# Kernel optimization log

Hardware: AMD Instinct MI355X
Metric: run time of the kernel (lower is better)

The kernel has to match this reference:

```python
import jax, jax.numpy as jnp
import numpy as np

N_NODES = 10000
DEG = 32          # random neighbors per node; +1 self loop (A + I in original)
BATCH = 2
F_IN = 128
D_EMB = 128


def _make_edges():
    # np.where on a dense (A+I) matrix yields edges sorted by source row;
    # we build the same sorted-by-src edge list directly.
    rng = np.random.default_rng(0)
    src = np.repeat(np.arange(N_NODES), DEG + 1)
    dst = rng.integers(0, N_NODES, size=N_NODES * (DEG + 1))
    dst[DEG::DEG + 1] = np.arange(N_NODES)  # guarantee self loops
    return np.stack([src, dst], axis=1).astype(np.int32)  # [E, 2]


def setup_inputs() -> dict:
    key = jax.random.key(0)
    k1, k2, k3 = jax.random.split(key, 3)
    inputs = jax.random.normal(k1, (BATCH, N_NODES, F_IN), jnp.float32)
    W = jax.random.normal(k2, (F_IN, D_EMB), jnp.float32) * 0.1
    W_attn = jax.random.normal(k3, (2 * D_EMB, 1), jnp.float32) * 0.1
    edges = jnp.asarray(_make_edges())
    return {"inputs": inputs, "W": W, "W_attn": W_attn, "edges": edges}


def reference(inputs, W, W_attn, edges):
    # inputs: [B, N, F]; W: [F, D]; W_attn: [2D, 1]; edges: [E, 2] (sorted by src)
    B, N, _ = inputs.shape
    D = W.shape[1]
    src, dst = edges[:, 0], edges[:, 1]

    h = inputs @ W  # [B, N, D] node_states_transformed

    # Original: gather [src,dst] feats, reshape to [B,E,2D], matmul W_attn.
    # Equivalent efficient form: split W_attn and project per node first.
    a_src, a_dst = W_attn[:D, 0], W_attn[D:, 0]
    s = h @ a_src  # [B, N]
    d = h @ a_dst  # [B, N]
    scores = jax.nn.leaky_relu(s[:, src] + d[:, dst], negative_slope=0.2)  # [B, E]
    scores = jnp.exp(jnp.clip(scores, -2.0, 2.0))

    # Faithful to original bug: denominator uses batch 0 only, shared across batch.
    denom = jax.ops.segment_sum(scores[0], src, num_segments=N)  # [N]
    # edges sorted by src => tf.repeat(denom, bincount(src)) == denom[src]
    attn = scores / denom[src][None, :]  # [B, E]

    msgs = h[:, dst] * attn[:, :, None]  # [B, E, D]
    # tf.unsorted_segment_sum with rank-2 segment_ids sums over batch AND edges.
    out = jax.ops.segment_sum(msgs.sum(axis=0), src, num_segments=N)  # [N, D]
    return jnp.broadcast_to(out[None], (B, N, D))
```

## Files before the change

kernel.cpp:

```cpp
#include <hip/hip_runtime.h>
#include <math.h>

#define N_NODES 10000
#define DEG1 33
#define D_EMB 128
#define F_IN 128
#define BATCH 2

typedef short s8v  __attribute__((ext_vector_type(8)));
typedef float f4v  __attribute__((ext_vector_type(4)));

static __device__ __forceinline__ unsigned short f2bf(float f) {
    unsigned int x = __float_as_uint(f);
    unsigned int r = (x + 0x7fffu + ((x >> 16) & 1u)) >> 16;
    return (unsigned short)r;
}
static __device__ __forceinline__ float rdlane_f(float v, int l) {
    return __uint_as_float((unsigned int)__builtin_amdgcn_readlane((int)__float_as_uint(v), l));
}

__global__ __launch_bounds__(256) void gat_prep_kernel(
    const float* __restrict__ W, unsigned short* __restrict__ wtf)
{
    const int c = blockIdx.x;
    const int t = threadIdx.x;
    __shared__ float xs[128 * 16];
    #pragma unroll
    for (int r = 0; r < 8; ++r) {
        const int k = r * 16 + (t >> 4);
        const int n = t & 15;
        xs[k * 16 + n] = W[k * 128 + c * 16 + n];
    }
    __syncthreads();
    const int s = t >> 6;
    const int l = t & 63;
    s8v frag;
    #pragma unroll
    for (int j = 0; j < 8; ++j) {
        const int k = s * 32 + (l >> 4) * 8 + j;
        frag[j] = (short)f2bf(xs[k * 16 + (l & 15)]);
    }
    *(s8v*)&wtf[(((size_t)c * 4 + s) * 64 + l) * 8] = frag;
}

__global__ __launch_bounds__(256) void gat_h_kernel(
    const float* __restrict__ X, const unsigned short* __restrict__ wtf,
    const float* __restrict__ Wattn,
    unsigned char* __restrict__ hb8, float* __restrict__ pk4, float* __restrict__ s2)
{
    __shared__ float lds_sd[2][2][2][16];
    __shared__ float lds_mx[2][2][16];
    const int wave = threadIdx.x >> 6;
    const int lane = threadIdx.x & 63;
    const int quad = lane >> 4;
    const int mrow = lane & 15;
    const int rg   = wave >> 1;
    const int half = wave & 1;
    const int row0 = (blockIdx.x * 2 + rg) * 16;

    f4v acc[4];
    #pragma unroll
    for (int cc = 0; cc < 4; ++cc) acc[cc] = (f4v){0.f, 0.f, 0.f, 0.f};

    const float* xrow = X + (size_t)(row0 + mrow) * F_IN;
    #pragma unroll
    for (int s = 0; s < 4; ++s) {
        const int k0 = s * 32 + quad * 8;
        const float4 xa = *(const float4*)&xrow[k0];
        const float4 xbv = *(const float4*)&xrow[k0 + 4];
        s8v a;
        a[0] = (short)f2bf(xa.x);  a[1] = (short)f2bf(xa.y);
        a[2] = (short)f2bf(xa.z);  a[3] = (short)f2bf(xa.w);
        a[4] = (short)f2bf(xbv.x); a[5] = (short)f2bf(xbv.y);
        a[6] = (short)f2bf(xbv.z); a[7] = (short)f2bf(xbv.w);
        #pragma unroll
        for (int cc = 0; cc < 4; ++cc) {
            const int c = half * 4 + cc;
            const s8v b = *(const s8v*)&wtf[(((size_t)c * 4 + s) * 64 + lane) * 8];
            acc[cc] = __builtin_amdgcn_mfma_f32_16x16x32_bf16(a, b, acc[cc], 0, 0, 0);
        }
    }

    float as[4], ad[4];
    #pragma unroll
    for (int cc = 0; cc < 4; ++cc) {
        as[cc] = Wattn[(half * 4 + cc) * 16 + mrow];
        ad[cc] = Wattn[D_EMB + (half * 4 + cc) * 16 + mrow];
    }
    #pragma unroll
    for (int r = 0; r < 4; ++r) {
        float sv = 0.f, dv = 0.f, mx = 0.f;
        #pragma unroll
        for (int cc = 0; cc < 4; ++cc) {
            sv = fmaf(acc[cc][r], as[cc], sv);
            dv = fmaf(acc[cc][r], ad[cc], dv);
            mx = fmaxf(mx, fabsf(acc[cc][r]));
        }
        #pragma unroll
        for (int off = 1; off < 16; off <<= 1) {
            sv += __shfl_xor(sv, off, 16);
            dv += __shfl_xor(dv, off, 16);
            mx = fmaxf(mx, __shfl_xor(mx, off, 16));
        }
        if (mrow == 0) {
            lds_sd[rg][half][0][quad * 4 + r] = sv;
            lds_sd[rg][half][1][quad * 4 + r] = dv;
            lds_mx[rg][half][quad * 4 + r] = mx;
        }
    }
    __syncthreads();

    const int b = (row0 >= N_NODES) ? 1 : 0;
    #pragma unroll
    for (int r = 0; r < 4; ++r) {
        const int qr = quad * 4 + r;
        const float mx = fmaxf(fmaxf(lds_mx[rg][0][qr], lds_mx[rg][1][qr]), 1e-20f);
        const float inv_s = 127.f / mx;
        const int n = (row0 + qr) - b * N_NODES;
        unsigned char* dst = &hb8[((size_t)n * 2 + b) * D_EMB + half * 64 + mrow];
        #pragma unroll
        for (int cc = 0; cc < 4; ++cc) {
            const float tq = fminf(fmaxf(acc[cc][r] * inv_s, -127.f), 127.f);
            dst[cc * 16] = (unsigned char)(__float2int_rn(tq) + 128);
        }
    }

    const int t = threadIdx.x;
    if (t < 32) {
        const int rg2 = t >> 4, r = t & 15;
        const int row = (blockIdx.x * 2 + rg2) * 16 + r;
        const int b2 = (row >= N_NODES) ? 1 : 0;
        const int n2 = row - b2 * N_NODES;
        const float s_full = lds_sd[rg2][0][0][r] + lds_sd[rg2][1][0][r];
        const float d_full = lds_sd[rg2][0][1][r] + lds_sd[rg2][1][1][r];
        const float mx = fmaxf(fmaxf(lds_mx[rg2][0][r], lds_mx[rg2][1][r]), 1e-20f);
        s2[(size_t)n2 * 2 + b2] = s_full;
        pk4[(size_t)n2 * 4 + b2] = d_full;
        pk4[(size_t)n2 * 4 + 2 + b2] = mx * (1.f / 127.f);
    }
}

__global__ __launch_bounds__(256) void gat_agg_kernel(
    const unsigned int* __restrict__ h4,
    const float* __restrict__ pk4, const float* __restrict__ s2,
    const int* __restrict__ edges, float* __restrict__ out)
{
    const int i = blockIdx.x * 4 + (threadIdx.x >> 6);
    const int lane = threadIdx.x & 63;

    int dstv = 0; float sc0 = 0.f, wS0 = 0.f, wS1 = 0.f;
    if (lane < DEG1) {
        dstv = edges[((size_t)i * DEG1 + lane) * 2 + 1];
        const float4 pk = *(const float4*)&pk4[(size_t)dstv * 4];
        const float s0 = s2[(size_t)i * 2];
        const float s1 = s2[(size_t)i * 2 + 1];
        float x0 = s0 + pk.x;
        float x1 = s1 + pk.y;
        x0 = (x0 >= 0.f) ? x0 : 0.2f * x0;
        x1 = (x1 >= 0.f) ? x1 : 0.2f * x1;
        sc0 = __expf(fminf(fmaxf(x0, -2.f), 2.f));
        const float sc1 = __expf(fminf(fmaxf(x1, -2.f), 2.f));
        wS0 = sc0 * pk.z;
        wS1 = sc1 * pk.w;
    }
    float dsum = sc0;
    #pragma unroll
    for (int off = 1; off < 64; off <<= 1) dsum += __shfl_xor(dsum, off, 64);
    const float inv = 1.f / dsum;
    wS0 *= inv;
    wS1 *= inv;
    float csum = wS0 + wS1;
    #pragma unroll
    for (int off = 1; off < 64; off <<= 1) csum += __shfl_xor(csum, off, 64);
    const float C = 128.f * csum;

    float4 acc = make_float4(0.f, 0.f, 0.f, 0.f);
    #pragma unroll
    for (int j = 0; j < DEG1; ++j) {
        const int   dd = __builtin_amdgcn_readlane(dstv, j);
        const float w0 = rdlane_f(wS0, j);
        const float w1 = rdlane_f(wS1, j);
        const float wgt = (lane < 32) ? w0 : w1;
        const unsigned int u = h4[(size_t)dd * 64 + lane];
        acc.x = fmaf(wgt, (float)(u & 0xffu), acc.x);
        acc.y = fmaf(wgt, (float)((u >> 8) & 0xffu), acc.y);
        acc.z = fmaf(wgt, (float)((u >> 16) & 0xffu), acc.z);
        acc.w = fmaf(wgt, (float)(u >> 24), acc.w);
    }
    float4 o;
    o.x = acc.x + __shfl_xor(acc.x, 32, 64) - C;
    o.y = acc.y + __shfl_xor(acc.y, 32, 64) - C;
    o.z = acc.z + __shfl_xor(acc.z, 32, 64) - C;
    o.w = acc.w + __shfl_xor(acc.w, 32, 64) - C;

    const int b  = lane >> 5;
    const int dl = lane & 31;
    *(float4*)&out[((size_t)b * N_NODES + i) * D_EMB + dl * 4] = o;
}

extern "C" void kernel_launch(void* const* d_in, const int* in_sizes, int n_in,
                              void* d_out, int out_size, void* d_ws, size_t ws_size,
                              hipStream_t stream) {
    const float* X     = (const float*)d_in[0];
    const float* W     = (const float*)d_in[1];
    const float* Wattn = (const float*)d_in[2];
    const int*   edges = (const int*)d_in[3];
    float* out = (float*)d_out;

    unsigned short* wtf = (unsigned short*)d_ws;
    unsigned char*  hb8 = (unsigned char*)(wtf + 16384);
    float* pk4 = (float*)(hb8 + (size_t)BATCH * N_NODES * D_EMB);
    float* s2  = pk4 + (size_t)N_NODES * 4;

    gat_prep_kernel<<<8, 256, 0, stream>>>(W, wtf);
    gat_h_kernel<<<625, 256, 0, stream>>>(X, wtf, Wattn, hb8, pk4, s2);
    gat_agg_kernel<<<N_NODES / 4, 256, 0, stream>>>((const unsigned int*)hb8, pk4, s2, edges, out);
}
```

Measured before the change: 86.38 us.

## Fuse prep, projection and aggregation into one cooperative persistent kernel

Merges the three launches into a single cooperative kernel. Each block converts W to bf16 MFMA fragments in shared memory, then loops persistently over projection tiles, performs a grid-wide sync, and then loops over nodes for the attention aggregation. The aim is to remove launch gaps and the global round trip of the weight fragments. In exchange every block redoes the W conversion, it adds a grid barrier, and it caps parallelism at the resident block count, which may lower memory-latency hiding in the gather phase.

```diff
diff --git a/kernel.cpp b/kernel.cpp
--- a/kernel.cpp
+++ b/kernel.cpp
@@ -1,4 +1,5 @@
 #include <hip/hip_runtime.h>
+#include <hip/hip_cooperative_groups.h>
 #include <math.h>
 
 #define N_NODES 10000
@@ -6,6 +7,9 @@
 #define D_EMB 128
 #define F_IN 128
 #define BATCH 2
+#define NTILES 625
+
+namespace cg = cooperative_groups;
 
 typedef short s8v  __attribute__((ext_vector_type(8)));
 typedef float f4v  __attribute__((ext_vector_type(4)));
@@ -19,183 +23,178 @@
     return __uint_as_float((unsigned int)__builtin_amdgcn_readlane((int)__float_as_uint(v), l));
 }
 
-__global__ __launch_bounds__(256) void gat_prep_kernel(
-    const float* __restrict__ W, unsigned short* __restrict__ wtf)
+__global__ __launch_bounds__(256, 2) void gat_fused_kernel(
+    const float* __restrict__ X, const float* __restrict__ W,
+    const float* __restrict__ Wattn, const int* __restrict__ edges,
+    float* __restrict__ out,
+    unsigned char* __restrict__ hb8, float* __restrict__ pk4, float* __restrict__ s2)
 {
-    const int c = blockIdx.x;
-    const int t = threadIdx.x;
-    __shared__ float xs[128 * 16];
+    __shared__ s8v   wfrag[2048];
+    __shared__ float lds_sd[2][2][2][16];
+    __shared__ float lds_mx[2][2][16];
+
+    const int t    = threadIdx.x;
+    const int wave = t >> 6;
+    const int lane = t & 63;
+    const int quad = lane >> 4;
+    const int mrow = lane & 15;
+
     #pragma unroll
-    for (int r = 0; r < 8; ++r) {
-        const int k = r * 16 + (t >> 4);
-        const int n = t & 15;
-        xs[k * 16 + n] = W[k * 128 + c * 16 + n];
+    for (int m = 0; m < 8; ++m) {
+        const int idx = t + 256 * m;
+        const int l = idx & 63;
+        const int s = (idx >> 6) & 3;
+        const int c = idx >> 8;
+        s8v f;
+        #pragma unroll
+        for (int j = 0; j < 8; ++j) {
+            const int k = s * 32 + (l >> 4) * 8 + j;
+            f[j] = (short)f2bf(W[k * 128 + c * 16 + (l & 15)]);
+        }
+        wfrag[idx] = f;
     }
     __syncthreads();
-    const int s = t >> 6;
-    const int l = t & 63;
-    s8v frag;
-    #pragma unroll
-    for (int j = 0; j < 8; ++j) {
-        const int k = s * 32 + (l >> 4) * 8 + j;
-        frag[j] = (short)f2bf(xs[k * 16 + (l & 15)]);
-    }
-    *(s8v*)&wtf[(((size_t)c * 4 + s) * 64 + l) * 8] = frag;
-}
-
-__global__ __launch_bounds__(256) void gat_h_kernel(
-    const float* __restrict__ X, const unsigned short* __restrict__ wtf,
-    const float* __restrict__ Wattn,
-    unsigned char* __restrict__ hb8, float* __restrict__ pk4, float* __restrict__ s2)
-{
-    __shared__ float lds_sd[2][2][2][16];
-    __shared__ float lds_mx[2][2][16];
-    const int wave = threadIdx.x >> 6;
-    const int lane = threadIdx.x & 63;
-    const int quad = lane >> 4;
-    const int mrow = lane & 15;
+
     const int rg   = wave >> 1;
     const int half = wave & 1;
-    const int row0 = (blockIdx.x * 2 + rg) * 16;
-
-    f4v acc[4];
-    #pragma unroll
-    for (int cc = 0; cc < 4; ++cc) acc[cc] = (f4v){0.f, 0.f, 0.f, 0.f};
-
-    const float* xrow = X + (size_t)(row0 + mrow) * F_IN;
-    #pragma unroll
-    for (int s = 0; s < 4; ++s) {
-        const int k0 = s * 32 + quad * 8;
-        const float4 xa = *(const float4*)&xrow[k0];
-        const float4 xbv = *(const float4*)&xrow[k0 + 4];
-        s8v a;
-        a[0] = (short)f2bf(xa.x);  a[1] = (short)f2bf(xa.y);
-        a[2] = (short)f2bf(xa.z);  a[3] = (short)f2bf(xa.w);
-        a[4] = (short)f2bf(xbv.x); a[5] = (short)f2bf(xbv.y);
-        a[6] = (short)f2bf(xbv.z); a[7] = (short)f2bf(xbv.w);
+    for (int vb = blockIdx.x; vb < NTILES; vb += gridDim.x) {
+        const int row0 = (vb * 2 + rg) * 16;
+
+        f4v acc[4];
+        #pragma unroll
+        for (int cc = 0; cc < 4; ++cc) acc[cc] = (f4v){0.f, 0.f, 0.f, 0.f};
+
+        const float* xrow = X + (size_t)(row0 + mrow) * F_IN;
+        #pragma unroll
+        for (int s = 0; s < 4; ++s) {
+            const int k0 = s * 32 + quad * 8;
+            const float4 xa  = *(const float4*)&xrow[k0];
+            const float4 xbv = *(const float4*)&xrow[k0 + 4];
+            s8v a;
+            a[0] = (short)f2bf(xa.x);  a[1] = (short)f2bf(xa.y);
+            a[2] = (short)f2bf(xa.z);  a[3] = (short)f2bf(xa.w);
+            a[4] = (short)f2bf(xbv.x); a[5] = (short)f2bf(xbv.y);
+            a[6] = (short)f2bf(xbv.z); a[7] = (short)f2bf(xbv.w);
+            #pragma unroll
+            for (int cc = 0; cc < 4; ++cc) {
+                const s8v b = wfrag[((half * 4 + cc) * 4 + s) * 64 + lane];
+                acc[cc] = __builtin_amdgcn_mfma_f32_16x16x32_bf16(a, b, acc[cc], 0, 0, 0);
+            }
+        }
+
+        float as[4], ad[4];
         #pragma unroll
         for (int cc = 0; cc < 4; ++cc) {
-            const int c = half * 4 + cc;
-            const s8v b = *(const s8v*)&wtf[(((size_t)c * 4 + s) * 64 + lane) * 8];
-            acc[cc] = __builtin_amdgcn_mfma_f32_16x16x32_bf16(a, b, acc[cc], 0, 0, 0);
-        }
+            as[cc] = Wattn[(half * 4 + cc) * 16 + mrow];
+            ad[cc] = Wattn[D_EMB + (half * 4 + cc) * 16 + mrow];
+        }
+        #pragma unroll
+        for (int r = 0; r < 4; ++r) {
+            float sv = 0.f, dv = 0.f, mx = 0.f;
+            #pragma unroll
+            for (int cc = 0; cc < 4; ++cc) {
+                sv = fmaf(acc[cc][r], as[cc], sv);
+                dv = fmaf(acc[cc][r], ad[cc], dv);
+                mx = fmaxf(mx, fabsf(acc[cc][r]));
+            }
+            #pragma unroll
+            for (int off = 1; off < 16; off <<= 1) {
+                sv += __shfl_xor(sv, off, 16);
+                dv += __shfl_xor(dv, off, 16);
+                mx = fmaxf(mx, __shfl_xor(mx, off, 16));
+            }
+            if (mrow == 0) {
+                lds_sd[rg][half][0][quad * 4 + r] = sv;
+                lds_sd[rg][half][1][quad * 4 + r] = dv;
+                lds_mx[rg][half][quad * 4 + r] = mx;
+            }
+        }
+        __syncthreads();
+
+        const int b = (row0 >= N_NODES) ? 1 : 0;
+        #pragma unroll
+        for (int r = 0; r < 4; ++r) {
+            const int qr = quad * 4 + r;
+            const float mx = fmaxf(fmaxf(lds_mx[rg][0][qr], lds_mx[rg][1][qr]), 1e-20f);
+            const float inv_s = 127.f / mx;
+            const int n = (row0 + qr) - b * N_NODES;
+            unsigned char* dst = &hb8[((size_t)n * 2 + b) * D_EMB + half * 64 + mrow];
+            #pragma unroll
+            for (int cc = 0; cc < 4; ++cc) {
+                const float tq = fminf(fmaxf(acc[cc][r] * inv_s, -127.f), 127.f);
+                dst[cc * 16] = (unsigned char)(__float2int_rn(tq) + 128);
+            }
+        }
+
+        if (t < 32) {
+            const int rg2 = t >> 4, r = t & 15;
+            const int row = (vb * 2 + rg2) * 16 + r;
+            const int b2 = (row >= N_NODES) ? 1 : 0;
+            const int n2 = row - b2 * N_NODES;
+            const float s_full = lds_sd[rg2][0][0][r] + lds_sd[rg2][1][0][r];
+            const float d_full = lds_sd[rg2][0][1][r] + lds_sd[rg2][1][1][r];
+            const float mx = fmaxf(fmaxf(lds_mx[rg2][0][r], lds_mx[rg2][1][r]), 1e-20f);
+            s2[(size_t)n2 * 2 + b2] = s_full;
+            pk4[(size_t)n2 * 4 + b2] = d_full;
+            pk4[(size_t)n2 * 4 + 2 + b2] = mx * (1.f / 127.f);
+        }
+        __syncthreads();
     }
 
-    float as[4], ad[4];
-    #pragma unroll
-    for (int cc = 0; cc < 4; ++cc) {
-        as[cc] = Wattn[(half * 4 + cc) * 16 + mrow];
-        ad[cc] = Wattn[D_EMB + (half * 4 + cc) * 16 + mrow];
+    __threadfence();
+    cg::this_grid().sync();
+
+    const int nwaves = gridDim.x * 4;
+    for (int i = blockIdx.x * 4 + wave; i < N_NODES; i += nwaves) {
+        int dstv = 0; float sc0 = 0.f, wS0 = 0.f, wS1 = 0.f;
+        if (lane < DEG1) {
+            dstv = edges[((size_t)i * DEG1 + lane) * 2 + 1];
+            const float4 pk = *(const float4*)&pk4[(size_t)dstv * 4];
+            const float2 ss = *(const float2*)&s2[(size_t)i * 2];
+            float x0 = ss.x + pk.x;
+            float x1 = ss.y + pk.y;
+            x0 = (x0 >= 0.f) ? x0 : 0.2f * x0;
+            x1 = (x1 >= 0.f) ? x1 : 0.2f * x1;
+            sc0 = __expf(fminf(fmaxf(x0, -2.f), 2.f));
+            const float sc1 = __expf(fminf(fmaxf(x1, -2.f), 2.f));
+            wS0 = sc0 * pk.z;
+            wS1 = sc1 * pk.w;
+        }
+        float dsum = sc0;
+        #pragma unroll
+        for (int off = 1; off < 64; off <<= 1) dsum += __shfl_xor(dsum, off, 64);
+        const float inv = 1.f / dsum;
+        wS0 *= inv;
+        wS1 *= inv;
+        float csum = wS0 + wS1;
+        #pragma unroll
+        for (int off = 1; off < 64; off <<= 1) csum += __shfl_xor(csum, off, 64);
+        const float C = 128.f * csum;
+
+        float4 acc = make_float4(0.f, 0.f, 0.f, 0.f);
+        const unsigned int* __restrict__ h4 = (const unsigned int*)hb8;
+        #pragma unroll
+        for (int j = 0; j < DEG1; ++j) {
+            const int   dd = __builtin_amdgcn_readlane(dstv, j);
+            const float w0 = rdlane_f(wS0, j);
+            const float w1 = rdlane_f(wS1, j);
+            const float wgt = (lane < 32) ? w0 : w1;
+            const unsigned int u = h4[(size_t)dd * 64 + lane];
+            acc.x = fmaf(wgt, (float)(u & 0xffu), acc.x);
+            acc.y = fmaf(wgt, (float)((u >> 8) & 0xffu), acc.y);
+            acc.z = fmaf(wgt, (float)((u >> 16) & 0xffu), acc.z);
+            acc.w = fmaf(wgt, (float)(u >> 24), acc.w);
+        }
+        float4 o;
+        o.x = acc.x + __shfl_xor(acc.x, 32, 64) - C;
+        o.y = acc.y + __shfl_xor(acc.y, 32, 64) - C;
+        o.z = acc.z + __shfl_xor(acc.z, 32, 64) - C;
+        o.w = acc.w + __shfl_xor(acc.w, 32, 64) - C;
+
+        const int b  = lane >> 5;
+        const int dl = lane & 31;
+        *(float4*)&out[((size_t)b * N_NODES + i) * D_EMB + dl * 4] = o;
     }
-    #pragma unroll
-    for (int r = 0; r < 4; ++r) {
-        float sv = 0.f, dv = 0.f, mx = 0.f;
-        #pragma unroll
-        for (int cc = 0; cc < 4; ++cc) {
-            sv = fmaf(acc[cc][r], as[cc], sv);
-            dv = fmaf(acc[cc][r], ad[cc], dv);
-            mx = fmaxf(mx, fabsf(acc[cc][r]));
-        }
-        #pragma unroll
-        for (int off = 1; off < 16; off <<= 1) {
-            sv += __shfl_xor(sv, off, 16);
-            dv += __shfl_xor(dv, off, 16);
-            mx = fmaxf(mx, __shfl_xor(mx, off, 16));
-        }
-        if (mrow == 0) {
-            lds_sd[rg][half][0][quad * 4 + r] = sv;
-            lds_sd[rg][half][1][quad * 4 + r] = dv;
-            lds_mx[rg][half][quad * 4 + r] = mx;
-        }
-    }
-    __syncthreads();
-
-    const int b = (row0 >= N_NODES) ? 1 : 0;
-    #pragma unroll
-    for (int r = 0; r < 4; ++r) {
-        const int qr = quad * 4 + r;
-        const float mx = fmaxf(fmaxf(lds_mx[rg][0][qr], lds_mx[rg][1][qr]), 1e-20f);
-        const float inv_s = 127.f / mx;
-        const int n = (row0 + qr) - b * N_NODES;
-        unsigned char* dst = &hb8[((size_t)n * 2 + b) * D_EMB + half * 64 + mrow];
-        #pragma unroll
-        for (int cc = 0; cc < 4; ++cc) {
-            const float tq = fminf(fmaxf(acc[cc][r] * inv_s, -127.f), 127.f);
-            dst[cc * 16] = (unsigned char)(__float2int_rn(tq) + 128);
-        }
-    }
-
-    const int t = threadIdx.x;
-    if (t < 32) {
-        const int rg2 = t >> 4, r = t & 15;
-        const int row = (blockIdx.x * 2 + rg2) * 16 + r;
-        const int b2 = (row >= N_NODES) ? 1 : 0;
-        const int n2 = row - b2 * N_NODES;
-        const float s_full = lds_sd[rg2][0][0][r] + lds_sd[rg2][1][0][r];
-        const float d_full = lds_sd[rg2][0][1][r] + lds_sd[rg2][1][1][r];
-        const float mx = fmaxf(fmaxf(lds_mx[rg2][0][r], lds_mx[rg2][1][r]), 1e-20f);
-        s2[(size_t)n2 * 2 + b2] = s_full;
-        pk4[(size_t)n2 * 4 + b2] = d_full;
-        pk4[(size_t)n2 * 4 + 2 + b2] = mx * (1.f / 127.f);
-    }
-}
-
-__global__ __launch_bounds__(256) void gat_agg_kernel(
-    const unsigned int* __restrict__ h4,
-    const float* __restrict__ pk4, const float* __restrict__ s2,
-    const int* __restrict__ edges, float* __restrict__ out)
-{
-    const int i = blockIdx.x * 4 + (threadIdx.x >> 6);
-    const int lane = threadIdx.x & 63;
-
-    int dstv = 0; float sc0 = 0.f, wS0 = 0.f, wS1 = 0.f;
-    if (lane < DEG1) {
-        dstv = edges[((size_t)i * DEG1 + lane) * 2 + 1];
-        const float4 pk = *(const float4*)&pk4[(size_t)dstv * 4];
-        const float s0 = s2[(size_t)i * 2];
-        const float s1 = s2[(size_t)i * 2 + 1];
-        float x0 = s0 + pk.x;
-        float x1 = s1 + pk.y;
-        x0 = (x0 >= 0.f) ? x0 : 0.2f * x0;
-        x1 = (x1 >= 0.f) ? x1 : 0.2f * x1;
-        sc0 = __expf(fminf(fmaxf(x0, -2.f), 2.f));
-        const float sc1 = __expf(fminf(fmaxf(x1, -2.f), 2.f));
-        wS0 = sc0 * pk.z;
-        wS1 = sc1 * pk.w;
-    }
-    float dsum = sc0;
-    #pragma unroll
-    for (int off = 1; off < 64; off <<= 1) dsum += __shfl_xor(dsum, off, 64);
-    const float inv = 1.f / dsum;
-    wS0 *= inv;
-    wS1 *= inv;
-    float csum = wS0 + wS1;
-    #pragma unroll
-    for (int off = 1; off < 64; off <<= 1) csum += __shfl_xor(csum, off, 64);
-    const float C = 128.f * csum;
-
-    float4 acc = make_float4(0.f, 0.f, 0.f, 0.f);
-    #pragma unroll
-    for (int j = 0; j < DEG1; ++j) {
-        const int   dd = __builtin_amdgcn_readlane(dstv, j);
-        const float w0 = rdlane_f(wS0, j);
-        const float w1 = rdlane_f(wS1, j);
-        const float wgt = (lane < 32) ? w0 : w1;
-        const unsigned int u = h4[(size_t)dd * 64 + lane];
-        acc.x = fmaf(wgt, (float)(u & 0xffu), acc.x);
-        acc.y = fmaf(wgt, (float)((u >> 8) & 0xffu), acc.y);
-        acc.z = fmaf(wgt, (float)((u >> 16) & 0xffu), acc.z);
-        acc.w = fmaf(wgt, (float)(u >> 24), acc.w);
-    }
-    float4 o;
-    o.x = acc.x + __shfl_xor(acc.x, 32, 64) - C;
-    o.y = acc.y + __shfl_xor(acc.y, 32, 64) - C;
-    o.z = acc.z + __shfl_xor(acc.z, 32, 64) - C;
-    o.w = acc.w + __shfl_xor(acc.w, 32, 64) - C;
-
-    const int b  = lane >> 5;
-    const int dl = lane & 31;
-    *(float4*)&out[((size_t)b * N_NODES + i) * D_EMB + dl * 4] = o;
 }
 
 extern "C" void kernel_launch(void* const* d_in, const int* in_sizes, int n_in,
@@ -207,12 +206,18 @@
     const int*   edges = (const int*)d_in[3];
     float* out = (float*)d_out;
 
-    unsigned short* wtf = (unsigned short*)d_ws;
-    unsigned char*  hb8 = (unsigned char*)(wtf + 16384);
+    unsigned char* hb8 = (unsigned char*)d_ws;
     float* pk4 = (float*)(hb8 + (size_t)BATCH * N_NODES * D_EMB);
     float* s2  = pk4 + (size_t)N_NODES * 4;
 
-    gat_prep_kernel<<<8, 256, 0, stream>>>(W, wtf);
-    gat_h_kernel<<<625, 256, 0, stream>>>(X, wtf, Wattn, hb8, pk4, s2);
-    gat_agg_kernel<<<N_NODES / 4, 256, 0, stream>>>((const unsigned int*)hb8, pk4, s2, edges, out);
-}
+    int occ = 0;
+    if (hipOccupancyMaxActiveBlocksPerMultiprocessor(&occ, gat_fused_kernel, 256, 0)
+            != hipSuccess || occ < 1) occ = 1;
+    if (occ > 4) occ = 4;
+    int grid = 256 * occ;
+
+    void* args[] = {(void*)&X, (void*)&W, (void*)&Wattn, (void*)&edges,
+                    (void*)&out, (void*)&hb8, (void*)&pk4, (void*)&s2};
+    hipLaunchCooperativeKernel((const void*)gat_fused_kernel, dim3(grid), dim3(256),
+                               args, 0, stream);
+}
```

Result: slower. 220.4 us (+155.2%).
